# Kernel tuning notes

Hardware: AMD Instinct MI355X
Metric: run time of the kernel (lower is better)

Reference implementation:

```python
import jax, jax.numpy as jnp
import numpy as np

N_NODES = 50000
N_HEDGES = 10000
N_MEMB = 800000
IN_SIZE = 256
HEADS = 4
OUT_SIZE = 64


def setup_inputs() -> dict:
    key = jax.random.key(0)
    k1, k2, k3, k4, k5 = jax.random.split(key, 5)
    x = jax.random.normal(k1, (N_NODES, IN_SIZE), dtype=jnp.float32)
    # Linear weight stored as [in, out*heads] so projection is x @ W (same math as torch Linear)
    W = jax.random.normal(k2, (IN_SIZE, OUT_SIZE * HEADS), dtype=jnp.float32) * (1.0 / np.sqrt(IN_SIZE))
    att_e = jax.random.normal(k3, (1, HEADS, OUT_SIZE), dtype=jnp.float32) * 0.1
    node_idx = jax.random.randint(k4, (N_MEMB,), 0, N_NODES, dtype=jnp.int64)
    hedge_idx = jax.random.randint(k5, (N_MEMB,), 0, N_HEDGES, dtype=jnp.int64)
    return {"x": x, "W": W, "att_e": att_e, "node_idx": node_idx,
            "hedge_idx": hedge_idx, "num_hyperedges": N_HEDGES}


def reference(x, W, att_e, node_idx, hedge_idx, num_hyperedges):
    # Dropout is treated as eval-mode identity.
    N = x.shape[0]
    H, D = att_e.shape[1], att_e.shape[2]
    xp = (x @ W).reshape(N, H, D)                                   # [N,H,D]
    # Stage 1: mean-aggregate node features into hyperedges (belongs-to)
    ones = jnp.ones(node_idx.shape[0], dtype=x.dtype)
    deg = jax.ops.segment_sum(ones, hedge_idx, num_segments=num_hyperedges)  # [E]
    he = jax.ops.segment_sum(xp[node_idx], hedge_idx, num_segments=num_hyperedges)
    he = he / jnp.maximum(deg, 1.0)[:, None, None]                  # [E,H,D]
    # Attention logit per hyperedge
    alpha_e = jax.nn.leaky_relu(jnp.sum(he * att_e, axis=-1), 0.2)  # [E,H]
    # Stage 2: edge_softmax over 'contains' edges grouped by destination node
    ae = alpha_e[hedge_idx]                                         # [M,H]
    mx = jax.ops.segment_max(ae, node_idx, num_segments=N)          # [N,H]
    ex = jnp.exp(ae - mx[node_idx])
    den = jax.ops.segment_sum(ex, node_idx, num_segments=N)         # [N,H]
    a = ex / den[node_idx]                                          # [M,H]
    # Attention-weighted scatter-sum of hyperedge features to nodes
    out = jax.ops.segment_sum(he[hedge_idx] * a[:, :, None], node_idx, num_segments=N)  # [N,H,D]
    return out.reshape(N, H * D)
```

## Files before the change

### kernel.cpp

```cpp
#include <hip/hip_runtime.h>
#include <hip/hip_fp16.h>
#include <math.h>

#define N_NODES  50000
#define N_HEDGES 10000
#define N_MEMB   800000
#define KIN      256
#define CH       256
#define HEADS    4
#define HCAP     160
#define NCAP     48

#define NCHUNK      125
#define CHUNK4      1600
#define XCVT_F4     3200000
#define XCVT_BLOCKS 1563
#define WCVT_BLOCKS 8
#define HED_W       2500
#define NOD_W       12500

typedef _Float16 half2v __attribute__((ext_vector_type(2)));

__device__ inline float2 h2f(unsigned u) {
    __half2 h = __builtin_bit_cast(__half2, u);
    return __half22float2(h);
}
__device__ inline unsigned f2h(float a, float b) {
    return __builtin_bit_cast(unsigned, __floats2half2_rn(a, b));
}
__device__ inline float4 u2tof4(uint2 u) {
    float2 lo = h2f(u.x), hi = h2f(u.y);
    return make_float4(lo.x, lo.y, hi.x, hi.y);
}
__device__ inline void acc4(float4& a, float4 f) {
    a.x += f.x; a.y += f.y; a.z += f.z; a.w += f.w;
}
__device__ inline void fmaU4(float4& A, float4& B, float w, uint4 g) {
    float2 f0 = h2f(g.x), f1 = h2f(g.y), f2 = h2f(g.z), f3 = h2f(g.w);
    A.x += w * f0.x; A.y += w * f0.y; A.z += w * f1.x; A.w += w * f1.y;
    B.x += w * f2.x; B.y += w * f2.y; B.z += w * f3.x; B.w += w * f3.y;
}
__device__ inline float fdot2w(half2v a, half2v b, float c) {
#if __has_builtin(__builtin_amdgcn_fdot2)
    return __builtin_amdgcn_fdot2(a, b, c, false);
#else
    return c + (float)a.x * (float)b.x + (float)a.y * (float)b.y;
#endif
}

__global__ __launch_bounds__(1024)
void k_hist_cvt(const int4* __restrict__ ni4, const int4* __restrict__ hi4,
                unsigned char* __restrict__ htab, unsigned char* __restrict__ ntab,
                const float4* __restrict__ x4, uint2* __restrict__ x16,
                const float* __restrict__ Wf, unsigned* __restrict__ Wp) {
    __shared__ unsigned sh[HED_W + NOD_W];
    int bid = blockIdx.x, tid = threadIdx.x;
    if (bid < NCHUNK) {
        int chunk = bid;
        for (int i = tid; i < HED_W + NOD_W; i += 1024) sh[i] = 0;
        __syncthreads();
        int base4 = chunk * CHUNK4;
        for (int i = tid; i < CHUNK4; i += 1024) {
            int4 e = hi4[base4 + i]; int4 n = ni4[base4 + i];
            #pragma unroll
            for (int k = 0; k < 4; k++) {
                int ev = (&e.x)[k], nv = (&n.x)[k];
                atomicAdd(&sh[ev >> 2], 1u << ((ev & 3) * 8));
                atomicAdd(&sh[HED_W + (nv >> 2)], 1u << ((nv & 3) * 8));
            }
        }
        __syncthreads();
        unsigned* hd = (unsigned*)(htab + (size_t)chunk * N_HEDGES);
        for (int i = tid; i < HED_W; i += 1024) hd[i] = sh[i];
        unsigned* nd = (unsigned*)(ntab + (size_t)chunk * N_NODES);
        for (int i = tid; i < NOD_W; i += 1024) nd[i] = sh[HED_W + i];
    } else if (bid < NCHUNK + XCVT_BLOCKS) {
        int i0 = (bid - NCHUNK) * 2048 + tid;
        #pragma unroll
        for (int r = 0; r < 2; r++) {
            int idx = i0 + r * 1024;
            if (idx < XCVT_F4) {
                float4 v = x4[idx];
                uint2 u; u.x = f2h(v.x, v.y); u.y = f2h(v.z, v.w);
                x16[idx] = u;
            }
        }
    } else {
        int tg = (bid - NCHUNK - XCVT_BLOCKS) * 1024 + tid;
        #pragma unroll
        for (int r = 0; r < 4; r++) {
            int wI = tg + r * 8192;
            int k2 = wI >> 8, c = wI & 255;
            Wp[wI] = f2h(Wf[(size_t)(2 * k2) * CH + c], Wf[(size_t)(2 * k2 + 1) * CH + c]);
        }
    }
}

__global__ __launch_bounds__(1024)
void k_scan(unsigned char* __restrict__ htab, unsigned char* __restrict__ ntab,
            int* __restrict__ hdeg, int* __restrict__ ndeg) {
    int b = blockIdx.x * 1024 + threadIdx.x;
    if (b < N_HEDGES) {
        int run = 0;
        for (int c = 0; c < NCHUNK; c++) {
            size_t idx = (size_t)c * N_HEDGES + b;
            int v = htab[idx];
            htab[idx] = (unsigned char)run;
            run += v;
        }
        hdeg[b] = run;
    } else if (b < N_HEDGES + N_NODES) {
        int nb = b - N_HEDGES;
        int run = 0;
        for (int c = 0; c < NCHUNK; c++) {
            size_t idx = (size_t)c * N_NODES + nb;
            int v = ntab[idx];
            ntab[idx] = (unsigned char)run;
            run += v;
        }
        ndeg[nb] = run;
    }
}

__global__ __launch_bounds__(1024)
void k_place(const int4* __restrict__ ni4, const int4* __restrict__ hi4,
             const unsigned char* __restrict__ htab, const unsigned char* __restrict__ ntab,
             int* __restrict__ hmem, int* __restrict__ nhedge) {
    __shared__ unsigned sh[HED_W + NOD_W];
    int bid = blockIdx.x, tid = threadIdx.x;
    int chunk = bid;
    for (int i = tid; i < HED_W + NOD_W; i += 1024) sh[i] = 0;
    __syncthreads();
    int base4 = chunk * CHUNK4;
    const unsigned char* hoff = htab + (size_t)chunk * N_HEDGES;
    const unsigned char* noff = ntab + (size_t)chunk * N_NODES;
    for (int i = tid; i < CHUNK4; i += 1024) {
        int4 e = hi4[base4 + i]; int4 n = ni4[base4 + i];
        #pragma unroll
        for (int k = 0; k < 4; k++) {
            int ev = (&e.x)[k], nv = (&n.x)[k];
            unsigned oldh = atomicAdd(&sh[ev >> 2], 1u << ((ev & 3) * 8));
            int rh = (int)((oldh >> ((ev & 3) * 8)) & 0xffu);
            int posh = (int)hoff[ev] + rh;
            if (posh < HCAP) hmem[(size_t)ev * HCAP + posh] = nv;
            unsigned oldn = atomicAdd(&sh[HED_W + (nv >> 2)], 1u << ((nv & 3) * 8));
            int rn = (int)((oldn >> ((nv & 3) * 8)) & 0xffu);
            int posn = (int)noff[nv] + rn;
            if (posn < NCAP) nhedge[(size_t)nv * NCAP + posn] = ev;
        }
    }
}

__global__ __launch_bounds__(256, 8)
void k_stage1(const int* __restrict__ hdeg, const int* __restrict__ hmem,
              const uint2* __restrict__ x16, const unsigned* __restrict__ Wp,
              const float* __restrict__ att, __half* __restrict__ he,
              float* __restrict__ alpha) {
    __shared__ int sidx[4][HCAP];
    __shared__ unsigned hxT[KIN / 2][4];
    int tid = threadIdx.x;
    int w = tid >> 6, lt = tid & 63;
    int e0 = blockIdx.x * 4;
    int e = e0 + w;
    int deg = hdeg[e];
    int degC = min(deg, HCAP);
    const int* ml = hmem + (size_t)e * HCAP;
    for (int j = lt; j < degC; j += 64) sidx[w][j] = ml[j];
    __syncthreads();
    float4 ac0 = {0,0,0,0}, ac1 = {0,0,0,0}, ac2 = {0,0,0,0}, ac3 = {0,0,0,0};
    for (int j = 0; j < degC; j += 8) {
        uint2 g[8];
        #pragma unroll
        for (int i = 0; i < 8; i++) {
            int jj = j + i; jj = jj < degC ? jj : degC - 1;
            g[i] = x16[(size_t)sidx[w][jj] * 64 + lt];
        }
        if (j + 0 < degC) acc4(ac0, u2tof4(g[0]));
        if (j + 1 < degC) acc4(ac1, u2tof4(g[1]));
        if (j + 2 < degC) acc4(ac2, u2tof4(g[2]));
        if (j + 3 < degC) acc4(ac3, u2tof4(g[3]));
        if (j + 4 < degC) acc4(ac0, u2tof4(g[4]));
        if (j + 5 < degC) acc4(ac1, u2tof4(g[5]));
        if (j + 6 < degC) acc4(ac2, u2tof4(g[6]));
        if (j + 7 < degC) acc4(ac3, u2tof4(g[7]));
    }
    float sx = (ac0.x + ac1.x) + (ac2.x + ac3.x);
    float sy = (ac0.y + ac1.y) + (ac2.y + ac3.y);
    float sz = (ac0.z + ac1.z) + (ac2.z + ac3.z);
    float sw = (ac0.w + ac1.w) + (ac2.w + ac3.w);
    float inv = deg > 0 ? 1.0f / (float)deg : 0.0f;
    hxT[2 * lt][w]     = f2h(sx * inv, sy * inv);
    hxT[2 * lt + 1][w] = f2h(sz * inv, sw * inv);
    __syncthreads();
    int c = tid;
    float a0 = 0.f, a1 = 0.f, a2 = 0.f, a3 = 0.f;
    for (int k2 = 0; k2 < KIN / 2; k2++) {
        unsigned wv = Wp[(size_t)k2 * CH + c];
        half2v wh = __builtin_bit_cast(half2v, wv);
        uint4 hq = *(const uint4*)&hxT[k2][0];
        a0 = fdot2w(__builtin_bit_cast(half2v, hq.x), wh, a0);
        a1 = fdot2w(__builtin_bit_cast(half2v, hq.y), wh, a1);
        a2 = fdot2w(__builtin_bit_cast(half2v, hq.z), wh, a2);
        a3 = fdot2w(__builtin_bit_cast(half2v, hq.w), wh, a3);
    }
    he[(size_t)(e0 + 0) * CH + c] = __float2half_rn(a0);
    he[(size_t)(e0 + 1) * CH + c] = __float2half_rn(a1);
    he[(size_t)(e0 + 2) * CH + c] = __float2half_rn(a2);
    he[(size_t)(e0 + 3) * CH + c] = __float2half_rn(a3);
    float av = att[c];
    float p0 = a0 * av, p1 = a1 * av, p2 = a2 * av, p3 = a3 * av;
    #pragma unroll
    for (int d = 32; d >= 1; d >>= 1) {
        p0 += __shfl_xor(p0, d, 64); p1 += __shfl_xor(p1, d, 64);
        p2 += __shfl_xor(p2, d, 64); p3 += __shfl_xor(p3, d, 64);
    }
    if (lt == 0) {
        alpha[(e0 + 0) * HEADS + w] = p0 > 0.f ? p0 : 0.2f * p0;
        alpha[(e0 + 1) * HEADS + w] = p1 > 0.f ? p1 : 0.2f * p1;
        alpha[(e0 + 2) * HEADS + w] = p2 > 0.f ? p2 : 0.2f * p2;
        alpha[(e0 + 3) * HEADS + w] = p3 > 0.f ? p3 : 0.2f * p3;
    }
}

__global__ __launch_bounds__(256, 8)
void k_stage2(const uint4* __restrict__ heu4, const float4* __restrict__ alpha4,
              const int* __restrict__ ndeg, const int* __restrict__ nhedge,
              float4* __restrict__ out) {
    __shared__ int   nh[4][NCAP];
    __shared__ float wl[4][4][NCAP];
    int tid = threadIdx.x;
    int w = tid >> 6, L = tid & 63;
    int half = L >> 5, q = L & 31;
    int n = blockIdx.x * 4 + w;
    int deg = min(ndeg[n], NCAP);
    const int* nl = nhedge + (size_t)n * NCAP;
    if (L < deg) nh[w][L] = nl[L];
    __syncthreads();
    float4 mx = make_float4(-INFINITY, -INFINITY, -INFINITY, -INFINITY);
    float4 w4 = make_float4(0.f, 0.f, 0.f, 0.f);
    float4 aj = mx;
    if (L < deg) { aj = alpha4[nh[w][L]]; mx = aj; }
    #pragma unroll
    for (int d = 32; d >= 1; d >>= 1) {
        mx.x = fmaxf(mx.x, __shfl_xor(mx.x, d, 64));
        mx.y = fmaxf(mx.y, __shfl_xor(mx.y, d, 64));
        mx.z = fmaxf(mx.z, __shfl_xor(mx.z, d, 64));
        mx.w = fmaxf(mx.w, __shfl_xor(mx.w, d, 64));
    }
    if (L < deg) {
        w4.x = __expf(aj.x - mx.x); w4.y = __expf(aj.y - mx.y);
        w4.z = __expf(aj.z - mx.z); w4.w = __expf(aj.w - mx.w);
        wl[w][0][L] = w4.x; wl[w][1][L] = w4.y;
        wl[w][2][L] = w4.z; wl[w][3][L] = w4.w;
    }
    float4 dn = w4;
    #pragma unroll
    for (int d = 32; d >= 1; d >>= 1) {
        dn.x += __shfl_xor(dn.x, d, 64);
        dn.y += __shfl_xor(dn.y, d, 64);
        dn.z += __shfl_xor(dn.z, d, 64);
        dn.w += __shfl_xor(dn.w, d, 64);
    }
    __syncthreads();
    int h = q >> 3;
    float den = h < 2 ? (h == 0 ? dn.x : dn.y) : (h == 2 ? dn.z : dn.w);
    float4 A = make_float4(0.f, 0.f, 0.f, 0.f);
    float4 B = make_float4(0.f, 0.f, 0.f, 0.f);
    if (deg > 0) {
        for (int j = 0; j < deg; j += 8) {
            uint4 g[4]; float wgt[4];
            #pragma unroll
            for (int i = 0; i < 4; i++) {
                int jj = j + 2 * i + half;
                int jc = jj < deg ? jj : deg - 1;
                wgt[i] = jj < deg ? wl[w][h][jc] : 0.f;
                g[i] = heu4[(size_t)nh[w][jc] * 32 + q];
            }
            #pragma unroll
            for (int i = 0; i < 4; i++) fmaU4(A, B, wgt[i], g[i]);
        }
    }
    A.x += __shfl_xor(A.x, 32, 64); A.y += __shfl_xor(A.y, 32, 64);
    A.z += __shfl_xor(A.z, 32, 64); A.w += __shfl_xor(A.w, 32, 64);
    B.x += __shfl_xor(B.x, 32, 64); B.y += __shfl_xor(B.y, 32, 64);
    B.z += __shfl_xor(B.z, 32, 64); B.w += __shfl_xor(B.w, 32, 64);
    if (half == 0) {
        if (deg > 0) {
            float inv = 1.0f / den;
            A.x *= inv; A.y *= inv; A.z *= inv; A.w *= inv;
            B.x *= inv; B.y *= inv; B.z *= inv; B.w *= inv;
        }
        out[(size_t)n * 64 + 2 * q]     = A;
        out[(size_t)n * 64 + 2 * q + 1] = B;
    }
}

extern "C" void kernel_launch(void* const* d_in, const int* in_sizes, int n_in,
                              void* d_out, int out_size, void* d_ws, size_t ws_size,
                              hipStream_t stream) {
    const float* x        = (const float*)d_in[0];
    const float* W        = (const float*)d_in[1];
    const float* att      = (const float*)d_in[2];
    const int*   node_idx = (const int*)d_in[3];
    const int*   hedge_idx= (const int*)d_in[4];
    float4* out4 = (float4*)d_out;

    char* ws = (char*)d_ws;
    size_t o = 0;
    auto alloc = [&](size_t b) { size_t r = o; o += (b + 255) & ~(size_t)255; return r; };
    float* alpha = (float*)(ws + alloc(sizeof(float) * (size_t)N_HEDGES * HEADS));
    unsigned* Wp = (unsigned*)(ws + alloc(sizeof(unsigned) * (KIN / 2) * CH));
    int*   hdeg  = (int*)(ws + alloc(sizeof(int) * N_HEDGES));
    int*   ndeg  = (int*)(ws + alloc(sizeof(int) * N_NODES));
    int*   hmem  = (int*)(ws + alloc(sizeof(int) * (size_t)N_HEDGES * HCAP));
    __half* he   = (__half*)(ws + alloc(sizeof(__half) * (size_t)N_HEDGES * CH));
    int*   nhedge = (int*)(ws + alloc(sizeof(int) * (size_t)N_NODES * NCAP));
    unsigned char* htab = (unsigned char*)(ws + alloc((size_t)NCHUNK * N_HEDGES));
    unsigned char* ntab = (unsigned char*)(ws + alloc((size_t)NCHUNK * N_NODES));
    if (o > ws_size) return;
    uint2* x16 = (uint2*)d_out;

    k_hist_cvt<<<NCHUNK + XCVT_BLOCKS + WCVT_BLOCKS, 1024, 0, stream>>>(
        (const int4*)node_idx, (const int4*)hedge_idx, htab, ntab,
        (const float4*)x, x16, W, Wp);
    k_scan<<<(N_HEDGES + N_NODES + 1023) / 1024, 1024, 0, stream>>>(htab, ntab, hdeg, ndeg);
    k_place<<<NCHUNK, 1024, 0, stream>>>(
        (const int4*)node_idx, (const int4*)hedge_idx, htab, ntab, hmem, nhedge);
    k_stage1<<<N_HEDGES / 4, 256, 0, stream>>>(hdeg, hmem, x16, Wp, att, he, alpha);
    k_stage2<<<N_NODES / 4, 256, 0, stream>>>((const uint4*)he, (const float4*)alpha,
                                              ndeg, nhedge, out4);
}
```

Before: 172.2 us.

## Merge five launches into two cooperative persistent kernels with grid syncs

The histogram/convert, scan and placement kernels are folded into one cooperative kernel, and stage1 and stage2 into a second one. Each uses grid-wide syncs in place of kernel boundaries, with grid-stride loops over the original block work. The aim is to remove launch gaps and inter-kernel drain between the dependent phases. The cost is a grid sized by occupancy rather than one block per work item, extra per-call host occupancy queries, and changed register limits on the fused kernels. If a cooperative launch fails, it falls back to the original five-kernel path.

```diff
diff --git a/kernel.cpp b/kernel.cpp
--- a/kernel.cpp
+++ b/kernel.cpp
@@ -1,6 +1,9 @@
 #include <hip/hip_runtime.h>
+#include <hip/hip_cooperative_groups.h>
 #include <hip/hip_fp16.h>
 #include <math.h>
+
+namespace cg = cooperative_groups;
 
 #define N_NODES  50000
 #define N_HEDGES 10000
@@ -11,13 +14,14 @@
 #define HCAP     160
 #define NCAP     48
 
-#define NCHUNK      125
-#define CHUNK4      1600
-#define XCVT_F4     3200000
+#define NCHUNK   125
+#define CHUNK4   1600
+#define XCVT_F4  3200000
 #define XCVT_BLOCKS 1563
 #define WCVT_BLOCKS 8
-#define HED_W       2500
-#define NOD_W       12500
+#define WP_N     32768
+#define HED_W    2500
+#define NOD_W    12500
 
 typedef _Float16 half2v __attribute__((ext_vector_type(2)));
 
@@ -48,93 +52,38 @@
 #endif
 }
 
-__global__ __launch_bounds__(1024)
-void k_hist_cvt(const int4* __restrict__ ni4, const int4* __restrict__ hi4,
-                unsigned char* __restrict__ htab, unsigned char* __restrict__ ntab,
-                const float4* __restrict__ x4, uint2* __restrict__ x16,
-                const float* __restrict__ Wf, unsigned* __restrict__ Wp) {
-    __shared__ unsigned sh[HED_W + NOD_W];
-    int bid = blockIdx.x, tid = threadIdx.x;
-    if (bid < NCHUNK) {
-        int chunk = bid;
-        for (int i = tid; i < HED_W + NOD_W; i += 1024) sh[i] = 0;
-        __syncthreads();
-        int base4 = chunk * CHUNK4;
-        for (int i = tid; i < CHUNK4; i += 1024) {
-            int4 e = hi4[base4 + i]; int4 n = ni4[base4 + i];
-            #pragma unroll
-            for (int k = 0; k < 4; k++) {
-                int ev = (&e.x)[k], nv = (&n.x)[k];
-                atomicAdd(&sh[ev >> 2], 1u << ((ev & 3) * 8));
-                atomicAdd(&sh[HED_W + (nv >> 2)], 1u << ((nv & 3) * 8));
-            }
-        }
-        __syncthreads();
-        unsigned* hd = (unsigned*)(htab + (size_t)chunk * N_HEDGES);
-        for (int i = tid; i < HED_W; i += 1024) hd[i] = sh[i];
-        unsigned* nd = (unsigned*)(ntab + (size_t)chunk * N_NODES);
-        for (int i = tid; i < NOD_W; i += 1024) nd[i] = sh[HED_W + i];
-    } else if (bid < NCHUNK + XCVT_BLOCKS) {
-        int i0 = (bid - NCHUNK) * 2048 + tid;
+__device__ inline void dev_hist_chunk(int chunk, const int4* ni4, const int4* hi4,
+                                      unsigned char* htab, unsigned char* ntab,
+                                      unsigned* sh, int tid) {
+    for (int i = tid; i < HED_W + NOD_W; i += blockDim.x) sh[i] = 0;
+    __syncthreads();
+    int base4 = chunk * CHUNK4;
+    for (int i = tid; i < CHUNK4; i += blockDim.x) {
+        int4 e = hi4[base4 + i]; int4 n = ni4[base4 + i];
         #pragma unroll
-        for (int r = 0; r < 2; r++) {
-            int idx = i0 + r * 1024;
-            if (idx < XCVT_F4) {
-                float4 v = x4[idx];
-                uint2 u; u.x = f2h(v.x, v.y); u.y = f2h(v.z, v.w);
-                x16[idx] = u;
-            }
-        }
-    } else {
-        int tg = (bid - NCHUNK - XCVT_BLOCKS) * 1024 + tid;
-        #pragma unroll
-        for (int r = 0; r < 4; r++) {
-            int wI = tg + r * 8192;
-            int k2 = wI >> 8, c = wI & 255;
-            Wp[wI] = f2h(Wf[(size_t)(2 * k2) * CH + c], Wf[(size_t)(2 * k2 + 1) * CH + c]);
-        }
-    }
-}
-
-__global__ __launch_bounds__(1024)
-void k_scan(unsigned char* __restrict__ htab, unsigned char* __restrict__ ntab,
-            int* __restrict__ hdeg, int* __restrict__ ndeg) {
-    int b = blockIdx.x * 1024 + threadIdx.x;
-    if (b < N_HEDGES) {
-        int run = 0;
-        for (int c = 0; c < NCHUNK; c++) {
-            size_t idx = (size_t)c * N_HEDGES + b;
-            int v = htab[idx];
-            htab[idx] = (unsigned char)run;
-            run += v;
-        }
-        hdeg[b] = run;
-    } else if (b < N_HEDGES + N_NODES) {
-        int nb = b - N_HEDGES;
-        int run = 0;
-        for (int c = 0; c < NCHUNK; c++) {
-            size_t idx = (size_t)c * N_NODES + nb;
-            int v = ntab[idx];
-            ntab[idx] = (unsigned char)run;
-            run += v;
-        }
-        ndeg[nb] = run;
-    }
-}
-
-__global__ __launch_bounds__(1024)
-void k_place(const int4* __restrict__ ni4, const int4* __restrict__ hi4,
-             const unsigned char* __restrict__ htab, const unsigned char* __restrict__ ntab,
-             int* __restrict__ hmem, int* __restrict__ nhedge) {
-    __shared__ unsigned sh[HED_W + NOD_W];
-    int bid = blockIdx.x, tid = threadIdx.x;
-    int chunk = bid;
-    for (int i = tid; i < HED_W + NOD_W; i += 1024) sh[i] = 0;
+        for (int k = 0; k < 4; k++) {
+            int ev = (&e.x)[k], nv = (&n.x)[k];
+            atomicAdd(&sh[ev >> 2], 1u << ((ev & 3) * 8));
+            atomicAdd(&sh[HED_W + (nv >> 2)], 1u << ((nv & 3) * 8));
+        }
+    }
+    __syncthreads();
+    unsigned* hd = (unsigned*)(htab + (size_t)chunk * N_HEDGES);
+    for (int i = tid; i < HED_W; i += blockDim.x) hd[i] = sh[i];
+    unsigned* nd = (unsigned*)(ntab + (size_t)chunk * N_NODES);
+    for (int i = tid; i < NOD_W; i += blockDim.x) nd[i] = sh[HED_W + i];
+    __syncthreads();
+}
+
+__device__ inline void dev_place_chunk(int chunk, const int4* ni4, const int4* hi4,
+                                       const unsigned char* htab, const unsigned char* ntab,
+                                       int* hmem, int* nhedge, unsigned* sh, int tid) {
+    for (int i = tid; i < HED_W + NOD_W; i += blockDim.x) sh[i] = 0;
     __syncthreads();
     int base4 = chunk * CHUNK4;
     const unsigned char* hoff = htab + (size_t)chunk * N_HEDGES;
     const unsigned char* noff = ntab + (size_t)chunk * N_NODES;
-    for (int i = tid; i < CHUNK4; i += 1024) {
+    for (int i = tid; i < CHUNK4; i += blockDim.x) {
         int4 e = hi4[base4 + i]; int4 n = ni4[base4 + i];
         #pragma unroll
         for (int k = 0; k < 4; k++) {
@@ -149,18 +98,40 @@
             if (posn < NCAP) nhedge[(size_t)nv * NCAP + posn] = ev;
         }
     }
-}
-
-__global__ __launch_bounds__(256, 8)
-void k_stage1(const int* __restrict__ hdeg, const int* __restrict__ hmem,
-              const uint2* __restrict__ x16, const unsigned* __restrict__ Wp,
-              const float* __restrict__ att, __half* __restrict__ he,
-              float* __restrict__ alpha) {
-    __shared__ int sidx[4][HCAP];
-    __shared__ unsigned hxT[KIN / 2][4];
-    int tid = threadIdx.x;
+    __syncthreads();
+}
+
+__device__ inline void dev_scan_one(int b, unsigned char* htab, unsigned char* ntab,
+                                    int* hdeg, int* ndeg) {
+    if (b < N_HEDGES) {
+        int run = 0;
+        for (int c = 0; c < NCHUNK; c++) {
+            size_t idx = (size_t)c * N_HEDGES + b;
+            int v = htab[idx];
+            htab[idx] = (unsigned char)run;
+            run += v;
+        }
+        hdeg[b] = run;
+    } else if (b < N_HEDGES + N_NODES) {
+        int nb = b - N_HEDGES;
+        int run = 0;
+        for (int c = 0; c < NCHUNK; c++) {
+            size_t idx = (size_t)c * N_NODES + nb;
+            int v = ntab[idx];
+            ntab[idx] = (unsigned char)run;
+            run += v;
+        }
+        ndeg[nb] = run;
+    }
+}
+
+__device__ inline void dev_stage1_group(int g, const int* hdeg, const int* hmem,
+                                        const uint2* x16, const unsigned* Wp,
+                                        const float* att, __half* he, float* alpha,
+                                        int (*sidx)[HCAP], unsigned (*hxT)[4],
+                                        int tid) {
     int w = tid >> 6, lt = tid & 63;
-    int e0 = blockIdx.x * 4;
+    int e0 = g * 4;
     int e = e0 + w;
     int deg = hdeg[e];
     int degC = min(deg, HCAP);
@@ -169,20 +140,20 @@
     __syncthreads();
     float4 ac0 = {0,0,0,0}, ac1 = {0,0,0,0}, ac2 = {0,0,0,0}, ac3 = {0,0,0,0};
     for (int j = 0; j < degC; j += 8) {
-        uint2 g[8];
+        uint2 gg[8];
         #pragma unroll
         for (int i = 0; i < 8; i++) {
             int jj = j + i; jj = jj < degC ? jj : degC - 1;
-            g[i] = x16[(size_t)sidx[w][jj] * 64 + lt];
-        }
-        if (j + 0 < degC) acc4(ac0, u2tof4(g[0]));
-        if (j + 1 < degC) acc4(ac1, u2tof4(g[1]));
-        if (j + 2 < degC) acc4(ac2, u2tof4(g[2]));
-        if (j + 3 < degC) acc4(ac3, u2tof4(g[3]));
-        if (j + 4 < degC) acc4(ac0, u2tof4(g[4]));
-        if (j + 5 < degC) acc4(ac1, u2tof4(g[5]));
-        if (j + 6 < degC) acc4(ac2, u2tof4(g[6]));
-        if (j + 7 < degC) acc4(ac3, u2tof4(g[7]));
+            gg[i] = x16[(size_t)sidx[w][jj] * 64 + lt];
+        }
+        if (j + 0 < degC) acc4(ac0, u2tof4(gg[0]));
+        if (j + 1 < degC) acc4(ac1, u2tof4(gg[1]));
+        if (j + 2 < degC) acc4(ac2, u2tof4(gg[2]));
+        if (j + 3 < degC) acc4(ac3, u2tof4(gg[3]));
+        if (j + 4 < degC) acc4(ac0, u2tof4(gg[4]));
+        if (j + 5 < degC) acc4(ac1, u2tof4(gg[5]));
+        if (j + 6 < degC) acc4(ac2, u2tof4(gg[6]));
+        if (j + 7 < degC) acc4(ac3, u2tof4(gg[7]));
     }
     float sx = (ac0.x + ac1.x) + (ac2.x + ac3.x);
     float sy = (ac0.y + ac1.y) + (ac2.y + ac3.y);
@@ -220,18 +191,16 @@
         alpha[(e0 + 2) * HEADS + w] = p2 > 0.f ? p2 : 0.2f * p2;
         alpha[(e0 + 3) * HEADS + w] = p3 > 0.f ? p3 : 0.2f * p3;
     }
-}
-
-__global__ __launch_bounds__(256, 8)
-void k_stage2(const uint4* __restrict__ heu4, const float4* __restrict__ alpha4,
-              const int* __restrict__ ndeg, const int* __restrict__ nhedge,
-              float4* __restrict__ out) {
-    __shared__ int   nh[4][NCAP];
-    __shared__ float wl[4][4][NCAP];
-    int tid = threadIdx.x;
+    __syncthreads();
+}
+
+__device__ inline void dev_stage2_group(int g, const uint4* heu4, const float4* alpha4,
+                                        const int* ndeg, const int* nhedge,
+                                        float4* out, int (*nh)[NCAP],
+                                        float (*wl)[4][NCAP], int tid) {
     int w = tid >> 6, L = tid & 63;
     int half = L >> 5, q = L & 31;
-    int n = blockIdx.x * 4 + w;
+    int n = g * 4 + w;
     int deg = min(ndeg[n], NCAP);
     const int* nl = nhedge + (size_t)n * NCAP;
     if (L < deg) nh[w][L] = nl[L];
@@ -268,16 +237,16 @@
     float4 B = make_float4(0.f, 0.f, 0.f, 0.f);
     if (deg > 0) {
         for (int j = 0; j < deg; j += 8) {
-            uint4 g[4]; float wgt[4];
+            uint4 gg[4]; float wgt[4];
             #pragma unroll
             for (int i = 0; i < 4; i++) {
                 int jj = j + 2 * i + half;
                 int jc = jj < deg ? jj : deg - 1;
                 wgt[i] = jj < deg ? wl[w][h][jc] : 0.f;
-                g[i] = heu4[(size_t)nh[w][jc] * 32 + q];
+                gg[i] = heu4[(size_t)nh[w][jc] * 32 + q];
             }
             #pragma unroll
-            for (int i = 0; i < 4; i++) fmaU4(A, B, wgt[i], g[i]);
+            for (int i = 0; i < 4; i++) fmaU4(A, B, wgt[i], gg[i]);
         }
     }
     A.x += __shfl_xor(A.x, 32, 64); A.y += __shfl_xor(A.y, 32, 64);
@@ -293,6 +262,127 @@
         out[(size_t)n * 64 + 2 * q]     = A;
         out[(size_t)n * 64 + 2 * q + 1] = B;
     }
+    __syncthreads();
+}
+
+__global__ __launch_bounds__(1024)
+void k_build(const int4* __restrict__ ni4, const int4* __restrict__ hi4,
+             unsigned char* __restrict__ htab, unsigned char* __restrict__ ntab,
+             const float4* __restrict__ x4, uint2* __restrict__ x16,
+             const float* __restrict__ Wf, unsigned* __restrict__ Wp,
+             int* __restrict__ hdeg, int* __restrict__ ndeg,
+             int* __restrict__ hmem, int* __restrict__ nhedge) {
+    cg::grid_group grid = cg::this_grid();
+    __shared__ unsigned sh[HED_W + NOD_W];
+    int bid = blockIdx.x, tid = threadIdx.x;
+    int nthr = gridDim.x * 1024;
+    int t = bid * 1024 + tid;
+    for (int chunk = bid; chunk < NCHUNK; chunk += gridDim.x)
+        dev_hist_chunk(chunk, ni4, hi4, htab, ntab, sh, tid);
+    for (int idx = t; idx < XCVT_F4; idx += nthr) {
+        float4 v = x4[idx];
+        uint2 u; u.x = f2h(v.x, v.y); u.y = f2h(v.z, v.w);
+        x16[idx] = u;
+    }
+    for (int wI = t; wI < WP_N; wI += nthr) {
+        int k2 = wI >> 8, c = wI & 255;
+        Wp[wI] = f2h(Wf[(size_t)(2 * k2) * CH + c], Wf[(size_t)(2 * k2 + 1) * CH + c]);
+    }
+    grid.sync();
+    for (int b = t; b < N_HEDGES + N_NODES; b += nthr)
+        dev_scan_one(b, htab, ntab, hdeg, ndeg);
+    grid.sync();
+    for (int chunk = bid; chunk < NCHUNK; chunk += gridDim.x)
+        dev_place_chunk(chunk, ni4, hi4, htab, ntab, hmem, nhedge, sh, tid);
+}
+
+union SMem {
+    struct { int sidx[4][HCAP]; unsigned hxT[KIN / 2][4]; } a;
+    struct { int nh[4][NCAP]; float wl[4][4][NCAP]; } b;
+};
+
+__global__ __launch_bounds__(256)
+void k_fused(const int* __restrict__ hdeg, const int* __restrict__ hmem,
+             const uint2* __restrict__ x16, const unsigned* __restrict__ Wp,
+             const float* __restrict__ att, __half* __restrict__ he,
+             float* __restrict__ alpha, const int* __restrict__ ndeg,
+             const int* __restrict__ nhedge, float4* __restrict__ out) {
+    cg::grid_group grid = cg::this_grid();
+    __shared__ SMem sm;
+    int tid = threadIdx.x;
+    for (int g = blockIdx.x; g < N_HEDGES / 4; g += gridDim.x)
+        dev_stage1_group(g, hdeg, hmem, x16, Wp, att, he, alpha,
+                         sm.a.sidx, sm.a.hxT, tid);
+    grid.sync();
+    for (int g = blockIdx.x; g < N_NODES / 4; g += gridDim.x)
+        dev_stage2_group(g, (const uint4*)he, (const float4*)alpha, ndeg, nhedge,
+                         out, sm.b.nh, sm.b.wl, tid);
+}
+
+__global__ __launch_bounds__(1024)
+void f_hist_cvt(const int4* __restrict__ ni4, const int4* __restrict__ hi4,
+                unsigned char* __restrict__ htab, unsigned char* __restrict__ ntab,
+                const float4* __restrict__ x4, uint2* __restrict__ x16,
+                const float* __restrict__ Wf, unsigned* __restrict__ Wp) {
+    __shared__ unsigned sh[HED_W + NOD_W];
+    int bid = blockIdx.x, tid = threadIdx.x;
+    if (bid < NCHUNK) {
+        dev_hist_chunk(bid, ni4, hi4, htab, ntab, sh, tid);
+    } else if (bid < NCHUNK + XCVT_BLOCKS) {
+        int i0 = (bid - NCHUNK) * 2048 + tid;
+        #pragma unroll
+        for (int r = 0; r < 2; r++) {
+            int idx = i0 + r * 1024;
+            if (idx < XCVT_F4) {
+                float4 v = x4[idx];
+                uint2 u; u.x = f2h(v.x, v.y); u.y = f2h(v.z, v.w);
+                x16[idx] = u;
+            }
+        }
+    } else {
+        int tg = (bid - NCHUNK - XCVT_BLOCKS) * 1024 + tid;
+        #pragma unroll
+        for (int r = 0; r < 4; r++) {
+            int wI = tg + r * 8192;
+            int k2 = wI >> 8, c = wI & 255;
+            Wp[wI] = f2h(Wf[(size_t)(2 * k2) * CH + c], Wf[(size_t)(2 * k2 + 1) * CH + c]);
+        }
+    }
+}
+
+__global__ __launch_bounds__(1024)
+void f_scan(unsigned char* __restrict__ htab, unsigned char* __restrict__ ntab,
+            int* __restrict__ hdeg, int* __restrict__ ndeg) {
+    int b = blockIdx.x * 1024 + threadIdx.x;
+    dev_scan_one(b, htab, ntab, hdeg, ndeg);
+}
+
+__global__ __launch_bounds__(1024)
+void f_place(const int4* __restrict__ ni4, const int4* __restrict__ hi4,
+             const unsigned char* __restrict__ htab, const unsigned char* __restrict__ ntab,
+             int* __restrict__ hmem, int* __restrict__ nhedge) {
+    __shared__ unsigned sh[HED_W + NOD_W];
+    dev_place_chunk(blockIdx.x, ni4, hi4, htab, ntab, hmem, nhedge, sh, threadIdx.x);
+}
+
+__global__ __launch_bounds__(256, 8)
+void f_stage1(const int* __restrict__ hdeg, const int* __restrict__ hmem,
+              const uint2* __restrict__ x16, const unsigned* __restrict__ Wp,
+              const float* __restrict__ att, __half* __restrict__ he,
+              float* __restrict__ alpha) {
+    __shared__ int sidx[4][HCAP];
+    __shared__ unsigned hxT[KIN / 2][4];
+    dev_stage1_group(blockIdx.x, hdeg, hmem, x16, Wp, att, he, alpha,
+                     sidx, hxT, threadIdx.x);
+}
+
+__global__ __launch_bounds__(256, 8)
+void f_stage2(const uint4* __restrict__ heu4, const float4* __restrict__ alpha4,
+              const int* __restrict__ ndeg, const int* __restrict__ nhedge,
+              float4* __restrict__ out) {
+    __shared__ int nh[4][NCAP];
+    __shared__ float wl[4][4][NCAP];
+    dev_stage2_group(blockIdx.x, heu4, alpha4, ndeg, nhedge, out, nh, wl, threadIdx.x);
 }
 
 extern "C" void kernel_launch(void* const* d_in, const int* in_sizes, int n_in,
@@ -320,13 +410,45 @@
     if (o > ws_size) return;
     uint2* x16 = (uint2*)d_out;
 
-    k_hist_cvt<<<NCHUNK + XCVT_BLOCKS + WCVT_BLOCKS, 1024, 0, stream>>>(
-        (const int4*)node_idx, (const int4*)hedge_idx, htab, ntab,
-        (const float4*)x, x16, W, Wp);
-    k_scan<<<(N_HEDGES + N_NODES + 1023) / 1024, 1024, 0, stream>>>(htab, ntab, hdeg, ndeg);
-    k_place<<<NCHUNK, 1024, 0, stream>>>(
-        (const int4*)node_idx, (const int4*)hedge_idx, htab, ntab, hmem, nhedge);
-    k_stage1<<<N_HEDGES / 4, 256, 0, stream>>>(hdeg, hmem, x16, Wp, att, he, alpha);
-    k_stage2<<<N_NODES / 4, 256, 0, stream>>>((const uint4*)he, (const float4*)alpha,
-                                              ndeg, nhedge, out4);
-}
+    const int4* ni4 = (const int4*)node_idx;
+    const int4* hi4 = (const int4*)hedge_idx;
+    const float4* x4 = (const float4*)x;
+
+    bool coop = true;
+    int dev = 0;
+    if (hipGetDevice(&dev) != hipSuccess) dev = 0;
+    int cu = 0;
+    if (hipDeviceGetAttribute(&cu, hipDeviceAttributeMultiprocessorCount, dev) != hipSuccess || cu <= 0)
+        cu = 256;
+    int nb1 = 0, nb2 = 0;
+    if (hipOccupancyMaxActiveBlocksPerMultiprocessor(&nb1, (const void*)k_build, 1024, 0) != hipSuccess || nb1 < 1)
+        coop = false;
+    if (hipOccupancyMaxActiveBlocksPerMultiprocessor(&nb2, (const void*)k_fused, 256, 0) != hipSuccess || nb2 < 1)
+        coop = false;
+    if (coop) {
+        int g1 = NCHUNK * 2; if (g1 > nb1 * cu) g1 = nb1 * cu;
+        int g2 = N_HEDGES / 4; if (g2 > nb2 * cu) g2 = nb2 * cu;
+        void* args1[] = { (void*)&ni4, (void*)&hi4, (void*)&htab, (void*)&ntab,
+                          (void*)&x4, (void*)&x16, (void*)&W, (void*)&Wp,
+                          (void*)&hdeg, (void*)&ndeg, (void*)&hmem, (void*)&nhedge };
+        hipError_t e = hipLaunchCooperativeKernel((void*)k_build, dim3(g1), dim3(1024),
+                                                  args1, 0, stream);
+        if (e == hipSuccess) {
+            void* args2[] = { (void*)&hdeg, (void*)&hmem, (void*)&x16, (void*)&Wp,
+                              (void*)&att, (void*)&he, (void*)&alpha, (void*)&ndeg,
+                              (void*)&nhedge, (void*)&out4 };
+            e = hipLaunchCooperativeKernel((void*)k_fused, dim3(g2), dim3(256),
+                                           args2, 0, stream);
+        }
+        if (e != hipSuccess) coop = false;
+    }
+    if (!coop) {
+        f_hist_cvt<<<NCHUNK + XCVT_BLOCKS + WCVT_BLOCKS, 1024, 0, stream>>>(
+            ni4, hi4, htab, ntab, x4, x16, W, Wp);
+        f_scan<<<(N_HEDGES + N_NODES + 1023) / 1024, 1024, 0, stream>>>(htab, ntab, hdeg, ndeg);
+        f_place<<<NCHUNK, 1024, 0, stream>>>(ni4, hi4, htab, ntab, hmem, nhedge);
+        f_stage1<<<N_HEDGES / 4, 256, 0, stream>>>(hdeg, hmem, x16, Wp, att, he, alpha);
+        f_stage2<<<N_NODES / 4, 256, 0, stream>>>((const uint4*)he, (const float4*)alpha,
+                                                  ndeg, nhedge, out4);
+    }
+}
```

Result: slower. 400.5 us (+132.5%).
